# Kernel optimization log

Hardware: AMD Instinct MI355X
Metric: run time of the kernel (lower is better)

## Reference

```python
import math
import jax, jax.numpy as jnp
import numpy as np

D_MODEL = 1024
HID = 128
H, NB = 16, 16


def setup_inputs() -> dict:
    key = jax.random.key(0)
    ks = jax.random.split(key, 8)
    B, L = 4, 4096
    theta_path = jax.random.normal(ks[0], (B, L, H, NB), dtype=jnp.float32)
    content_emb = jax.random.normal(ks[1], (B, L, D_MODEL), dtype=jnp.float32)
    # measure_head params (PyTorch Linear default init: U(-1/sqrt(fan_in), 1/sqrt(fan_in)))
    s1 = 1.0 / math.sqrt(D_MODEL)
    s2 = 1.0 / math.sqrt(HID)
    W1 = jax.random.uniform(ks[2], (D_MODEL, HID), minval=-s1, maxval=s1, dtype=jnp.float32)
    b1 = jax.random.uniform(ks[3], (HID,), minval=-s1, maxval=s1, dtype=jnp.float32)
    W2 = jax.random.uniform(ks[4], (HID, H * NB), minval=-s2, maxval=s2, dtype=jnp.float32)
    b2 = jax.random.uniform(ks[5], (H * NB,), minval=-s2, maxval=s2, dtype=jnp.float32)
    log_Pi = jnp.zeros((H, NB), dtype=jnp.float32)
    log_R = jnp.zeros((H, NB), dtype=jnp.float32)
    return {"theta_path": theta_path, "content_emb": content_emb, "W1": W1, "b1": b1,
            "W2": W2, "b2": b2, "log_Pi": log_Pi, "log_R": log_R}


def _affine_scan(alpha, u):
    # d_t = alpha_t * d_{t-1} + u_t, d_0 = u_0 (zero initial state), scan over axis=1 (L)
    def combine(left, right):
        a_l, u_l = left
        a_r, u_r = right
        return a_l * a_r, a_r * u_l + u_r
    _, d = jax.lax.associative_scan(combine, (alpha, u), axis=1)
    return d


def reference(theta_path, content_emb, W1, b1, W2, b2, log_Pi, log_R):
    B, L, _, _ = theta_path.shape
    h = jax.nn.gelu(content_emb @ W1 + b1, approximate=False)  # [B,L,128], exact GELU as torch
    z = jnp.pi * jnp.tanh((h @ W2 + b2).reshape(B, L, H, NB))
    diff = z - theta_path
    nu = jnp.arctan2(jnp.sin(diff), jnp.cos(diff))  # wrapped angle residual
    Pi = jnp.exp(log_Pi)[None, None]  # [1,1,H,NB]
    R = jnp.exp(log_R)[None, None]
    K = Pi / jnp.maximum(Pi + R, 1e-08)
    Kf = jnp.broadcast_to(K, (B, L, H, NB))
    alpha = 1.0 - Kf
    u = Kf * nu
    d = _affine_scan(alpha, u)
    return (theta_path + d,
            jnp.broadcast_to(Pi, (B, L, H, NB)),
            Kf,
            jnp.broadcast_to(R, (B, L, H, NB)))
```

## Files before the change

### kernel.cpp

```cpp
#include <hip/hip_runtime.h>
#include <math.h>

#define MTOT  16384
#define DM    1024
#define HIDN  128
#define HNB   256
#define NBAT  4
#define CLK   32
#define NBLK  512
#define CPB   128

typedef _Float16 v8h __attribute__((ext_vector_type(8)));
typedef float    v4f __attribute__((ext_vector_type(4)));
#define MFMA16(a,b,c) __builtin_amdgcn_mfma_f32_16x16x32_f16((a),(b),(c),0,0,0)

#define W1TILE  16384
#define W2BASE  524288
#define W2TILE  32768
#define BLOB_BYTES 655360

#define RAWOFF 0
#define W1OFF  16384
#define HHOFF  0
#define HLOFF  8192
#define ZOFF   16384
#define SMEMSZ 65536

#define VMCNT_(N) asm volatile("s_waitcnt vmcnt(" #N ")" ::: "memory")
#define VMCNT(N) VMCNT_(N)
#define BARRIER() do { asm volatile("s_waitcnt lgkmcnt(0)" ::: "memory"); \
                       __builtin_amdgcn_s_barrier(); } while (0)

typedef const __attribute__((address_space(1))) void* gas1_t;
typedef __attribute__((address_space(3))) void* las3_t;

__device__ __forceinline__ void gld16(const void* g, void* l) {
    __builtin_amdgcn_global_load_lds((gas1_t)g, (las3_t)l, 16, 0, 0);
}

__global__ __launch_bounds__(256) void k_prep(
    const float* __restrict__ W1,
    const float* __restrict__ W2,
    char* __restrict__ blobs)
{
    __shared__ float lds[32][260];
    const int t = threadIdx.x, blk = blockIdx.x;
    if (blk < 32) {
        const int k0 = blk * 32;
        #pragma unroll
        for (int i = 0; i < 4; ++i) {
            int j = t + i * 256;
            int k = j >> 5, n4 = (j & 31) << 2;
            *(float4*)&lds[k][n4] = *(const float4*)&W1[(size_t)(k0 + k) * HIDN + n4];
        }
        __syncthreads();
        const int fl = t & 63, np = t >> 6;
        const int kb = (fl >> 4) * 8;
        #pragma unroll
        for (int fi = 0; fi < 2; ++fi) {
            const int col = 32 * np + 16 * fi + (fl & 15);
            union { _Float16 h[8]; int4 v; } H, L;
            #pragma unroll
            for (int e = 0; e < 8; ++e) {
                float v = lds[kb + e][col];
                _Float16 hh = (_Float16)v;
                H.h[e] = hh;
                L.h[e] = (_Float16)((v - (float)hh) * 4096.f);
            }
            char* d = blobs + blk * W1TILE + np * 2048 + fi * 1024 + fl * 16;
            *(int4*)d = H.v;
            *(int4*)(d + 8192) = L.v;
        }
    } else {
        const int ks = blk - 32, k0 = ks * 32;
        #pragma unroll
        for (int i = 0; i < 8; ++i) {
            int j = t + i * 256;
            int k = j >> 6, n4 = (j & 63) << 2;
            *(float4*)&lds[k][n4] = *(const float4*)&W2[(size_t)(k0 + k) * HNB + n4];
        }
        __syncthreads();
        const int fl = t & 63, cg0 = t >> 6;
        const int kb = (fl >> 4) * 8;
        #pragma unroll
        for (int i = 0; i < 4; ++i) {
            const int cg = cg0 * 4 + i;
            const int col = cg * 16 + (fl & 15);
            union { _Float16 h[8]; int4 v; } H, L;
            #pragma unroll
            for (int e = 0; e < 8; ++e) {
                float v = lds[kb + e][col];
                _Float16 hh = (_Float16)v;
                H.h[e] = hh;
                L.h[e] = (_Float16)((v - (float)hh) * 4096.f);
            }
            char* d = blobs + W2BASE + ks * W2TILE + cg * 1024 + fl * 16;
            *(int4*)d = H.v;
            *(int4*)(d + 16384) = L.v;
        }
    }
}

__global__ __launch_bounds__(512, 4) void k_mega(
    const float* __restrict__ A,
    const float* __restrict__ theta,
    const float* __restrict__ b1, const float* __restrict__ b2,
    const float* __restrict__ logPi, const float* __restrict__ logR,
    const char* __restrict__ blobs,
    float* __restrict__ out0, float* __restrict__ out2,
    float* fill1, float* fill3,
    float* carry, int cstride)
{
    __shared__ __attribute__((aligned(16))) char smem[SMEMSZ];

    const int tid  = threadIdx.x;
    const int blk  = blockIdx.x;
    const int m0   = blk * CLK;
    const int lane = tid & 63;
    const int wid  = tid >> 6;
    const int ln15 = lane & 15;
    const int q    = lane >> 4;
    const int np   = wid & 3;
    const int mh   = wid >> 2;

    const int mh_s = wid >> 1, half_s = wid & 1;
    const float* aSrc = A + (size_t)(m0 + 16 * mh_s + ln15) * DM + q * 8 + half_s * 4;
    const int rawDst = wid * 1024 + lane * 16;

    const int wq = wid & 3;
    const char* wSrc = blobs + wq * 2048 + (size_t)lane * 16;
    const int   wDst = wq * 2048 + lane * 16;

    v4f acc1[2], acc2[2];
    acc1[0] = acc1[1] = (v4f){0.f, 0.f, 0.f, 0.f};
    acc2[0] = acc2[1] = (v4f){0.f, 0.f, 0.f, 0.f};

#define STEP(KT, AV, WV, DO_RAW, DO_W) do { \
    if (wid < 4) { \
        if (DO_RAW) gld16(aSrc + (size_t)((KT) + 3) * 32, \
                          smem + RAWOFF + (((KT) + 3) & 3) * 4096 + rawDst); \
    } else if (DO_W) { \
        const char* ws_ = wSrc + (size_t)((KT) + 2) * W1TILE; \
        char* wd_ = smem + W1OFF + (((KT) + 2) % 3) * 16384 + wDst; \
        gld16(ws_, wd_);             gld16(ws_ + 1024, wd_ + 1024); \
        gld16(ws_ + 8192, wd_ + 8192); gld16(ws_ + 9216, wd_ + 9216); \
    } \
    { \
        const char* rawb = smem + RAWOFF + ((KT) & 3) * 4096 + mh * 2048 + lane * 16; \
        v4f lo = *(const v4f*)rawb; \
        v4f hi = *(const v4f*)(rawb + 1024); \
        const char* wbB = smem + W1OFF + ((KT) % 3) * 16384 + np * 2048 + lane * 16; \
        v8h wh0 = *(const v8h*)(wbB); \
        v8h wh1 = *(const v8h*)(wbB + 1024); \
        v8h wl0 = *(const v8h*)(wbB + 8192); \
        v8h wl1 = *(const v8h*)(wbB + 9216); \
        v8h ah, al; \
        _Pragma("unroll") \
        for (int e_ = 0; e_ < 4; ++e_) { \
            _Float16 t0_ = (_Float16)lo[e_]; \
            ah[e_] = t0_; \
            al[e_] = (_Float16)((lo[e_] - (float)t0_) * 4096.f); \
            _Float16 t1_ = (_Float16)hi[e_]; \
            ah[e_ + 4] = t1_; \
            al[e_ + 4] = (_Float16)((hi[e_] - (float)t1_) * 4096.f); \
        } \
        acc1[0] = MFMA16(ah, wh0, acc1[0]); \
        acc2[0] = MFMA16(ah, wl0, acc2[0]); \
        acc2[0] = MFMA16(al, wh0, acc2[0]); \
        acc1[1] = MFMA16(ah, wh1, acc1[1]); \
        acc2[1] = MFMA16(ah, wl1, acc2[1]); \
        acc2[1] = MFMA16(al, wh1, acc2[1]); \
    } \
    if (wid < 4) { VMCNT(AV); } else { VMCNT(WV); } \
    BARRIER(); \
} while (0)

    if (wid < 4) {
        gld16(aSrc,      smem + RAWOFF + 0 * 4096 + rawDst);
        gld16(aSrc + 32, smem + RAWOFF + 1 * 4096 + rawDst);
        gld16(aSrc + 64, smem + RAWOFF + 2 * 4096 + rawDst);
        VMCNT(2);
    } else {
        #pragma unroll
        for (int t2 = 0; t2 < 2; ++t2) {
            const char* ws_ = wSrc + (size_t)t2 * W1TILE;
            char* wd_ = smem + W1OFF + t2 * 16384 + wDst;
            gld16(ws_, wd_);               gld16(ws_ + 1024, wd_ + 1024);
            gld16(ws_ + 8192, wd_ + 8192); gld16(ws_ + 9216, wd_ + 9216);
        }
        VMCNT(4);
    }
    BARRIER();

    STEP(0,2,4,1,1);  STEP(1,2,4,1,1);  STEP(2,2,4,1,1);  STEP(3,2,4,1,1);
    STEP(4,2,4,1,1);  STEP(5,2,4,1,1);  STEP(6,2,4,1,1);  STEP(7,2,4,1,1);
    STEP(8,2,4,1,1);  STEP(9,2,4,1,1);  STEP(10,2,4,1,1); STEP(11,2,4,1,1);
    STEP(12,2,4,1,1); STEP(13,2,4,1,1); STEP(14,2,4,1,1); STEP(15,2,4,1,1);
    STEP(16,2,4,1,1); STEP(17,2,4,1,1); STEP(18,2,4,1,1); STEP(19,2,4,1,1);
    STEP(20,2,4,1,1); STEP(21,2,4,1,1); STEP(22,2,4,1,1); STEP(23,2,4,1,1);
    STEP(24,2,4,1,1); STEP(25,2,4,1,1); STEP(26,2,4,1,1); STEP(27,2,4,1,1);
    STEP(28,2,4,1,1); STEP(29,1,4,0,1); STEP(30,0,0,0,0); STEP(31,0,0,0,0);

    const float inv = 1.f / 4096.f;
    #pragma unroll
    for (int ni = 0; ni < 2; ++ni) {
        const int colH = 32 * np + 16 * ni + ln15;
        const float bv = b1[colH];
        const int qH = (colH >> 3) & 3;
        const int eH = colH & 7;
        #pragma unroll
        for (int r = 0; r < 4; ++r) {
            float y = acc1[ni][r] + acc2[ni][r] * inv + bv;
            float h = 0.5f * y * (1.f + erff(y * 0.70710678118654752f));
            _Float16 hh = (_Float16)h;
            _Float16 hl = (_Float16)((h - (float)hh) * 4096.f);
            const int fl = (4 * q + r) + 16 * qH;
            const int byte_ = mh * 4096 + np * 1024 + fl * 16 + eH * 2;
            *(_Float16*)(smem + HHOFF + byte_) = hh;
            *(_Float16*)(smem + HLOFF + byte_) = hl;
        }
    }
    BARRIER();

    v4f c1[4], c2[4];
    #pragma unroll
    for (int i = 0; i < 4; ++i) {
        c1[i] = (v4f){0.f, 0.f, 0.f, 0.f};
        c2[i] = (v4f){0.f, 0.f, 0.f, 0.f};
    }
    #pragma unroll
    for (int ks = 0; ks < 4; ++ks) {
        v8h hh = *(const v8h*)(smem + HHOFF + mh * 4096 + ks * 1024 + lane * 16);
        v8h hl = *(const v8h*)(smem + HLOFF + mh * 4096 + ks * 1024 + lane * 16);
        #pragma unroll
        for (int ni = 0; ni < 4; ++ni) {
            const char* wp = blobs + W2BASE + (size_t)ks * W2TILE
                           + (4 * np + ni) * 1024 + (size_t)lane * 16;
            v8h w2h = *(const v8h*)wp;
            v8h w2l = *(const v8h*)(wp + 16384);
            c1[ni] = MFMA16(hh, w2h, c1[ni]);
            c2[ni] = MFMA16(hh, w2l, c2[ni]);
            c2[ni] = MFMA16(hl, w2h, c2[ni]);
        }
    }

    #pragma unroll
    for (int ni = 0; ni < 4; ++ni) {
        const int col = 64 * np + 16 * ni + ln15;
        const float bv = b2[col];
        #pragma unroll
        for (int r = 0; r < 4; ++r) {
            const int row = 16 * mh + 4 * q + r;
            float y2 = c1[ni][r] + c2[ni][r] * inv + bv;
            *(float*)(smem + ZOFF + row * 1040 + col * 4) =
                3.14159265358979323846f * tanhf(y2);
        }
    }
    BARRIER();

    if (tid < 256) {
        const int c = tid;
        const float Pi = expf(logPi[c]);
        const float Rr = expf(logR[c]);
        const float Kc = Pi / fmaxf(Pi + Rr, 1e-8f);
        const float alpha = 1.f - Kc;
        float d = 0.f;
        float tv[2][16];
        #pragma unroll
        for (int i = 0; i < 16; ++i)
            tv[0][i] = theta[(size_t)(m0 + i) * HNB + c];
        #pragma unroll
        for (int g = 0; g < 2; ++g) {
            if (g < 1) {
                #pragma unroll
                for (int i = 0; i < 16; ++i)
                    tv[1][i] = theta[(size_t)(m0 + 16 + i) * HNB + c];
            }
            float sv[16];
            #pragma unroll
            for (int i = 0; i < 16; ++i) {
                float z = *(const float*)(smem + ZOFF + (g * 16 + i) * 1040 + c * 4);
                float diff = z - tv[g][i];
                float kq = rintf(diff * 0.15915494309189533577f);
                float nu = (float)((double)diff - (double)kq * 6.283185307179586476925286766559);
                d = fmaf(alpha, d, Kc * nu);
                sv[i] = tv[g][i] + d;
            }
            #pragma unroll
            for (int i = 0; i < 16; ++i)
                out0[(size_t)(m0 + g * 16 + i) * HNB + c] = sv[i];
        }
        carry[(size_t)blk * cstride + c] = d;
    } else {
        const int c = tid - 256;
        const float Pi = expf(logPi[c]);
        const float Rr = expf(logR[c]);
        const float Kc = Pi / fmaxf(Pi + Rr, 1e-8f);
        if (fill1) {
            #pragma unroll 4
            for (int i = 0; i < CLK; ++i) {
                size_t idx = (size_t)(m0 + i) * HNB + c;
                out2[idx]  = Kc;
                fill1[idx] = Pi;
                fill3[idx] = Rr;
            }
        } else {
            #pragma unroll 4
            for (int i = 0; i < CLK; ++i)
                out2[(size_t)(m0 + i) * HNB + c] = Kc;
        }
    }
#undef STEP
}

__global__ __launch_bounds__(256) void k_cscan(
    const float* __restrict__ logPi, const float* __restrict__ logR,
    float* carry, int cstride)
{
    const int c = threadIdx.x, b = blockIdx.x;
    const float Pi = expf(logPi[c]);
    const float Rr = expf(logR[c]);
    const float alpha = 1.f - Pi / fmaxf(Pi + Rr, 1e-8f);
    float A32 = alpha;
    #pragma unroll
    for (int i = 0; i < 5; ++i) A32 *= A32;
    float D = 0.f;
    for (int s0 = 0; s0 < CPB; s0 += 16) {
        float a[16];
        #pragma unroll
        for (int j = 0; j < 16; ++j)
            a[j] = carry[(size_t)(b * CPB + s0 + j) * cstride + c];
        #pragma unroll
        for (int j = 0; j < 16; ++j) {
            carry[(size_t)(b * CPB + s0 + j) * cstride + c] = D;
            D = fmaf(A32, D, a[j]);
        }
    }
}

__global__ __launch_bounds__(256) void k_apply(
    const float* __restrict__ logPi, const float* __restrict__ logR,
    float* __restrict__ out0, float* out1, float* out3,
    const float* carry, int cstride, int do_fills)
{
    const int blk = blockIdx.x;
    const int c = threadIdx.x;
    const float Pi = expf(logPi[c]);
    const float Rr = expf(logR[c]);
    const float Kc = Pi / fmaxf(Pi + Rr, 1e-8f);
    const float alpha = 1.f - Kc;
    float D = carry[(size_t)blk * cstride + c];
    float w = alpha * D;
    const size_t base = (size_t)blk * (CLK * HNB) + c;
    if (do_fills) {
        #pragma unroll 4
        for (int i = 0; i < CLK; ++i) {
            size_t idx = base + (size_t)i * HNB;
            out0[idx] += w;
            out1[idx] = Pi;
            out3[idx] = Rr;
            w *= alpha;
        }
    } else {
        #pragma unroll 4
        for (int i = 0; i < CLK; ++i) {
            size_t idx = base + (size_t)i * HNB;
            out0[idx] += w;
            w *= alpha;
        }
    }
}

extern "C" void kernel_launch(void* const* d_in, const int* in_sizes, int n_in,
                              void* d_out, int out_size, void* d_ws, size_t ws_size,
                              hipStream_t stream) {
    const float* theta   = (const float*)d_in[0];
    const float* content = (const float*)d_in[1];
    const float* W1      = (const float*)d_in[2];
    const float* b1      = (const float*)d_in[3];
    const float* W2      = (const float*)d_in[4];
    const float* b2      = (const float*)d_in[5];
    const float* logPi   = (const float*)d_in[6];
    const float* logR    = (const float*)d_in[7];

    float* out  = (float*)d_out;
    float* out0 = out;
    float* out1 = out + (size_t)MTOT * HNB;
    float* out2 = out + (size_t)2 * MTOT * HNB;
    float* out3 = out + (size_t)3 * MTOT * HNB;

    const size_t carry_bytes = (size_t)NBLK * 256 * 4;
    const size_t need = carry_bytes + BLOB_BYTES;
    float* carry; int cstride, do_fills; char* blobs;
    float *f1, *f3;
    if (ws_size >= need) {
        carry   = (float*)d_ws;
        cstride = 256;
        blobs   = (char*)d_ws + carry_bytes;
        f1 = out1; f3 = out3; do_fills = 0;
    } else {
        carry   = out3;
        cstride = CLK * HNB;
        blobs   = (char*)out1;
        f1 = nullptr; f3 = nullptr; do_fills = 1;
    }

    hipLaunchKernelGGL(k_prep, dim3(36), dim3(256), 0, stream, W1, W2, blobs);
    hipLaunchKernelGGL(k_mega, dim3(NBLK), dim3(512), 0, stream,
                       content, theta, b1, b2, logPi, logR, blobs,
                       out0, out2, f1, f3, carry, cstride);
    hipLaunchKernelGGL(k_cscan, dim3(NBAT), dim3(256), 0, stream,
                       logPi, logR, carry, cstride);
    hipLaunchKernelGGL(k_apply, dim3(NBLK), dim3(256), 0, stream,
                       logPi, logR, out0, out1, out3, carry, cstride, do_fills);
}
```

Baseline: 62.61 us.

## Double row-chunk to 64 and switch fused MLP to 32x32 MFMA tiles

Result: faster. 61.34 us (-2.0%).

```diff
diff --git a/kernel.cpp b/kernel.cpp
--- a/kernel.cpp
+++ b/kernel.cpp
@@ -6,25 +6,26 @@
 #define HIDN  128
 #define HNB   256
 #define NBAT  4
-#define CLK   32
-#define NBLK  512
-#define CPB   128
-
-typedef _Float16 v8h __attribute__((ext_vector_type(8)));
-typedef float    v4f __attribute__((ext_vector_type(4)));
-#define MFMA16(a,b,c) __builtin_amdgcn_mfma_f32_16x16x32_f16((a),(b),(c),0,0,0)
-
-#define W1TILE  16384
-#define W2BASE  524288
-#define W2TILE  32768
+#define CLK   64
+#define NBLK  256
+#define CPB   64
+
+typedef _Float16 v8h  __attribute__((ext_vector_type(8)));
+typedef float    v4f  __attribute__((ext_vector_type(4)));
+typedef float    v16f __attribute__((ext_vector_type(16)));
+#define MFMA32(a,b,c) __builtin_amdgcn_mfma_f32_32x32x16_f16((a),(b),(c),0,0,0)
+
+#define W1TILE 16384
+#define W2BASE 524288
+#define W2TILE 32768
 #define BLOB_BYTES 655360
 
 #define RAWOFF 0
-#define W1OFF  16384
+#define W1OFF  49152
 #define HHOFF  0
-#define HLOFF  8192
-#define ZOFF   16384
-#define SMEMSZ 65536
+#define HLOFF  16384
+#define ZOFF   49152
+#define SMEMSZ 115712
 
 #define VMCNT_(N) asm volatile("s_waitcnt vmcnt(" #N ")" ::: "memory")
 #define VMCNT(N) VMCNT_(N)
@@ -54,20 +55,18 @@
             *(float4*)&lds[k][n4] = *(const float4*)&W1[(size_t)(k0 + k) * HIDN + n4];
         }
         __syncthreads();
-        const int fl = t & 63, np = t >> 6;
-        const int kb = (fl >> 4) * 8;
-        #pragma unroll
-        for (int fi = 0; fi < 2; ++fi) {
-            const int col = 32 * np + 16 * fi + (fl & 15);
+        const int l = t & 63, fi = t >> 6;
+        #pragma unroll
+        for (int kb = 0; kb < 2; ++kb) {
             union { _Float16 h[8]; int4 v; } H, L;
             #pragma unroll
             for (int e = 0; e < 8; ++e) {
-                float v = lds[kb + e][col];
+                float v = lds[kb * 16 + (l >> 5) * 8 + e][32 * fi + (l & 31)];
                 _Float16 hh = (_Float16)v;
                 H.h[e] = hh;
                 L.h[e] = (_Float16)((v - (float)hh) * 4096.f);
             }
-            char* d = blobs + blk * W1TILE + np * 2048 + fi * 1024 + fl * 16;
+            char* d = blobs + blk * W1TILE + (fi * 2 + kb) * 1024 + l * 16;
             *(int4*)d = H.v;
             *(int4*)(d + 8192) = L.v;
         }
@@ -80,28 +79,29 @@
             *(float4*)&lds[k][n4] = *(const float4*)&W2[(size_t)(k0 + k) * HNB + n4];
         }
         __syncthreads();
-        const int fl = t & 63, cg0 = t >> 6;
-        const int kb = (fl >> 4) * 8;
-        #pragma unroll
-        for (int i = 0; i < 4; ++i) {
-            const int cg = cg0 * 4 + i;
-            const int col = cg * 16 + (fl & 15);
-            union { _Float16 h[8]; int4 v; } H, L;
+        const int l = t & 63, fi = t >> 6;
+        #pragma unroll
+        for (int jj = 0; jj < 2; ++jj) {
+            const int cg = fi * 2 + jj;
             #pragma unroll
-            for (int e = 0; e < 8; ++e) {
-                float v = lds[kb + e][col];
-                _Float16 hh = (_Float16)v;
-                H.h[e] = hh;
-                L.h[e] = (_Float16)((v - (float)hh) * 4096.f);
+            for (int kb = 0; kb < 2; ++kb) {
+                union { _Float16 h[8]; int4 v; } H, L;
+                #pragma unroll
+                for (int e = 0; e < 8; ++e) {
+                    float v = lds[kb * 16 + (l >> 5) * 8 + e][32 * cg + (l & 31)];
+                    _Float16 hh = (_Float16)v;
+                    H.h[e] = hh;
+                    L.h[e] = (_Float16)((v - (float)hh) * 4096.f);
+                }
+                char* d = blobs + W2BASE + ks * W2TILE + (cg * 2 + kb) * 1024 + l * 16;
+                *(int4*)d = H.v;
+                *(int4*)(d + 16384) = L.v;
             }
-            char* d = blobs + W2BASE + ks * W2TILE + cg * 1024 + fl * 16;
-            *(int4*)d = H.v;
-            *(int4*)(d + 16384) = L.v;
-        }
-    }
-}
-
-__global__ __launch_bounds__(512, 4) void k_mega(
+        }
+    }
+}
+
+__global__ __launch_bounds__(512, 2) void k_mega(
     const float* __restrict__ A,
     const float* __restrict__ theta,
     const float* __restrict__ b1, const float* __restrict__ b2,
@@ -118,140 +118,133 @@
     const int m0   = blk * CLK;
     const int lane = tid & 63;
     const int wid  = tid >> 6;
-    const int ln15 = lane & 15;
-    const int q    = lane >> 4;
+    const int c5   = lane & 31;
+    const int g    = lane >> 5;
     const int np   = wid & 3;
-    const int mh   = wid >> 2;
-
-    const int mh_s = wid >> 1, half_s = wid & 1;
-    const float* aSrc = A + (size_t)(m0 + 16 * mh_s + ln15) * DM + q * 8 + half_s * 4;
-    const int rawDst = wid * 1024 + lane * 16;
-
-    const int wq = wid & 3;
-    const char* wSrc = blobs + wq * 2048 + (size_t)lane * 16;
-    const int   wDst = wq * 2048 + lane * 16;
-
-    v4f acc1[2], acc2[2];
-    acc1[0] = acc1[1] = (v4f){0.f, 0.f, 0.f, 0.f};
-    acc2[0] = acc2[1] = (v4f){0.f, 0.f, 0.f, 0.f};
-
-#define STEP(KT, AV, WV, DO_RAW, DO_W) do { \
-    if (wid < 4) { \
-        if (DO_RAW) gld16(aSrc + (size_t)((KT) + 3) * 32, \
-                          smem + RAWOFF + (((KT) + 3) & 3) * 4096 + rawDst); \
-    } else if (DO_W) { \
-        const char* ws_ = wSrc + (size_t)((KT) + 2) * W1TILE; \
-        char* wd_ = smem + W1OFF + (((KT) + 2) % 3) * 16384 + wDst; \
-        gld16(ws_, wd_);             gld16(ws_ + 1024, wd_ + 1024); \
-        gld16(ws_ + 8192, wd_ + 8192); gld16(ws_ + 9216, wd_ + 9216); \
+    const int rh   = wid >> 2;
+
+    const int rh_s = wid >> 2, kb_s = (wid >> 1) & 1, half_s = wid & 1;
+    const float* aSrc = A + (size_t)(m0 + 32 * rh_s + c5) * DM
+                      + kb_s * 16 + g * 8 + half_s * 4;
+    const int rawPiece = wid * 1024 + lane * 16;
+
+    const char* wSrc = blobs + (size_t)wid * 4096 + (size_t)lane * 16;
+    const int   wDst = W1OFF + wid * 4096 + lane * 16;
+
+    v16f acc1, acc2;
+    #pragma unroll
+    for (int i = 0; i < 16; ++i) { acc1[i] = 0.f; acc2[i] = 0.f; }
+
+    gld16(aSrc,      smem + RAWOFF + 0 * 8192 + rawPiece);
+    gld16(aSrc + 32, smem + RAWOFF + 1 * 8192 + rawPiece);
+    #pragma unroll
+    for (int i = 0; i < 4; ++i)
+        gld16(wSrc + i * 1024, smem + wDst + i * 1024);
+    gld16(aSrc + 64, smem + RAWOFF + 2 * 8192 + rawPiece);
+    gld16(aSrc + 96, smem + RAWOFF + 3 * 8192 + rawPiece);
+    VMCNT(2);
+    BARRIER();
+
+#define PHASE(P) do { \
+    if ((P) <= 14) { \
+        const char* ws_ = wSrc + (size_t)(2 * (P) + 2) * W1TILE; \
+        char* wd_ = smem + (((P) + 1) & 1) * 32768 + wDst; \
+        gld16(ws_, wd_);               gld16(ws_ + 1024, wd_ + 1024); \
+        gld16(ws_ + 2048, wd_ + 2048); gld16(ws_ + 3072, wd_ + 3072); \
     } \
-    { \
-        const char* rawb = smem + RAWOFF + ((KT) & 3) * 4096 + mh * 2048 + lane * 16; \
-        v4f lo = *(const v4f*)rawb; \
-        v4f hi = *(const v4f*)(rawb + 1024); \
-        const char* wbB = smem + W1OFF + ((KT) % 3) * 16384 + np * 2048 + lane * 16; \
-        v8h wh0 = *(const v8h*)(wbB); \
-        v8h wh1 = *(const v8h*)(wbB + 1024); \
-        v8h wl0 = *(const v8h*)(wbB + 8192); \
-        v8h wl1 = *(const v8h*)(wbB + 9216); \
-        v8h ah, al; \
+    if ((P) <= 13) { \
+        gld16(aSrc + (size_t)(2 * (P) + 4) * 32, \
+              smem + RAWOFF + ((2 * (P) + 4) % 6) * 8192 + rawPiece); \
+        gld16(aSrc + (size_t)(2 * (P) + 5) * 32, \
+              smem + RAWOFF + ((2 * (P) + 5) % 6) * 8192 + rawPiece); \
+    } \
+    _Pragma("unroll") \
+    for (int t_ = 0; t_ < 2; ++t_) { \
+        const char* slot_ = smem + RAWOFF + ((2 * (P) + t_) % 6) * 8192; \
+        const char* wb_ = smem + W1OFF + ((P) & 1) * 32768 + t_ * 16384; \
         _Pragma("unroll") \
-        for (int e_ = 0; e_ < 4; ++e_) { \
-            _Float16 t0_ = (_Float16)lo[e_]; \
-            ah[e_] = t0_; \
-            al[e_] = (_Float16)((lo[e_] - (float)t0_) * 4096.f); \
-            _Float16 t1_ = (_Float16)hi[e_]; \
-            ah[e_ + 4] = t1_; \
-            al[e_ + 4] = (_Float16)((hi[e_] - (float)t1_) * 4096.f); \
+        for (int kb_ = 0; kb_ < 2; ++kb_) { \
+            v4f lo_ = *(const v4f*)(slot_ + (rh * 4 + kb_ * 2) * 1024 + lane * 16); \
+            v4f hi_ = *(const v4f*)(slot_ + (rh * 4 + kb_ * 2 + 1) * 1024 + lane * 16); \
+            v8h ah_, al_; \
+            _Pragma("unroll") \
+            for (int e_ = 0; e_ < 4; ++e_) { \
+                _Float16 t0_ = (_Float16)lo_[e_]; \
+                ah_[e_] = t0_; \
+                al_[e_] = (_Float16)((lo_[e_] - (float)t0_) * 4096.f); \
+                _Float16 t1_ = (_Float16)hi_[e_]; \
+                ah_[e_ + 4] = t1_; \
+                al_[e_ + 4] = (_Float16)((hi_[e_] - (float)t1_) * 4096.f); \
+            } \
+            v8h wh_ = *(const v8h*)(wb_ + (np * 2 + kb_) * 1024 + lane * 16); \
+            v8h wl_ = *(const v8h*)(wb_ + 8192 + (np * 2 + kb_) * 1024 + lane * 16); \
+            acc1 = MFMA32(ah_, wh_, acc1); \
+            acc2 = MFMA32(ah_, wl_, acc2); \
+            acc2 = MFMA32(al_, wh_, acc2); \
         } \
-        acc1[0] = MFMA16(ah, wh0, acc1[0]); \
-        acc2[0] = MFMA16(ah, wl0, acc2[0]); \
-        acc2[0] = MFMA16(al, wh0, acc2[0]); \
-        acc1[1] = MFMA16(ah, wh1, acc1[1]); \
-        acc2[1] = MFMA16(ah, wl1, acc2[1]); \
-        acc2[1] = MFMA16(al, wh1, acc2[1]); \
     } \
-    if (wid < 4) { VMCNT(AV); } else { VMCNT(WV); } \
+    if ((P) <= 13)      { VMCNT(2); } \
+    else if ((P) == 14) { VMCNT(0); } \
     BARRIER(); \
 } while (0)
 
-    if (wid < 4) {
-        gld16(aSrc,      smem + RAWOFF + 0 * 4096 + rawDst);
-        gld16(aSrc + 32, smem + RAWOFF + 1 * 4096 + rawDst);
-        gld16(aSrc + 64, smem + RAWOFF + 2 * 4096 + rawDst);
-        VMCNT(2);
-    } else {
-        #pragma unroll
-        for (int t2 = 0; t2 < 2; ++t2) {
-            const char* ws_ = wSrc + (size_t)t2 * W1TILE;
-            char* wd_ = smem + W1OFF + t2 * 16384 + wDst;
-            gld16(ws_, wd_);               gld16(ws_ + 1024, wd_ + 1024);
-            gld16(ws_ + 8192, wd_ + 8192); gld16(ws_ + 9216, wd_ + 9216);
-        }
-        VMCNT(4);
-    }
-    BARRIER();
-
-    STEP(0,2,4,1,1);  STEP(1,2,4,1,1);  STEP(2,2,4,1,1);  STEP(3,2,4,1,1);
-    STEP(4,2,4,1,1);  STEP(5,2,4,1,1);  STEP(6,2,4,1,1);  STEP(7,2,4,1,1);
-    STEP(8,2,4,1,1);  STEP(9,2,4,1,1);  STEP(10,2,4,1,1); STEP(11,2,4,1,1);
-    STEP(12,2,4,1,1); STEP(13,2,4,1,1); STEP(14,2,4,1,1); STEP(15,2,4,1,1);
-    STEP(16,2,4,1,1); STEP(17,2,4,1,1); STEP(18,2,4,1,1); STEP(19,2,4,1,1);
-    STEP(20,2,4,1,1); STEP(21,2,4,1,1); STEP(22,2,4,1,1); STEP(23,2,4,1,1);
-    STEP(24,2,4,1,1); STEP(25,2,4,1,1); STEP(26,2,4,1,1); STEP(27,2,4,1,1);
-    STEP(28,2,4,1,1); STEP(29,1,4,0,1); STEP(30,0,0,0,0); STEP(31,0,0,0,0);
+    PHASE(0);  PHASE(1);  PHASE(2);  PHASE(3);
+    PHASE(4);  PHASE(5);  PHASE(6);  PHASE(7);
+    PHASE(8);  PHASE(9);  PHASE(10); PHASE(11);
+    PHASE(12); PHASE(13); PHASE(14); PHASE(15);
+#undef PHASE
 
     const float inv = 1.f / 4096.f;
-    #pragma unroll
-    for (int ni = 0; ni < 2; ++ni) {
-        const int colH = 32 * np + 16 * ni + ln15;
-        const float bv = b1[colH];
-        const int qH = (colH >> 3) & 3;
-        const int eH = colH & 7;
-        #pragma unroll
-        for (int r = 0; r < 4; ++r) {
-            float y = acc1[ni][r] + acc2[ni][r] * inv + bv;
+    {
+        const int col = 32 * np + c5;
+        const float bv = b1[col];
+        const int kb2 = col >> 4;
+        const int fragBase = (rh * 8 + kb2) * 1024 + ((col & 15) >> 3) * 512
+                           + (col & 7) * 2;
+        #pragma unroll
+        for (int reg = 0; reg < 16; ++reg) {
+            const int row32 = (reg & 3) + 8 * (reg >> 2) + 4 * g;
+            float y = acc1[reg] + acc2[reg] * inv + bv;
             float h = 0.5f * y * (1.f + erff(y * 0.70710678118654752f));
             _Float16 hh = (_Float16)h;
             _Float16 hl = (_Float16)((h - (float)hh) * 4096.f);
-            const int fl = (4 * q + r) + 16 * qH;
-            const int byte_ = mh * 4096 + np * 1024 + fl * 16 + eH * 2;
-            *(_Float16*)(smem + HHOFF + byte_) = hh;
-            *(_Float16*)(smem + HLOFF + byte_) = hl;
+            *(_Float16*)(smem + HHOFF + fragBase + row32 * 16) = hh;
+            *(_Float16*)(smem + HLOFF + fragBase + row32 * 16) = hl;
         }
     }
     BARRIER();
 
-    v4f c1[4], c2[4];
-    #pragma unroll
-    for (int i = 0; i < 4; ++i) {
-        c1[i] = (v4f){0.f, 0.f, 0.f, 0.f};
-        c2[i] = (v4f){0.f, 0.f, 0.f, 0.f};
-    }
-    #pragma unroll
-    for (int ks = 0; ks < 4; ++ks) {
-        v8h hh = *(const v8h*)(smem + HHOFF + mh * 4096 + ks * 1024 + lane * 16);
-        v8h hl = *(const v8h*)(smem + HLOFF + mh * 4096 + ks * 1024 + lane * 16);
-        #pragma unroll
-        for (int ni = 0; ni < 4; ++ni) {
+    v16f d1[2], d2[2];
+    #pragma unroll
+    for (int i = 0; i < 16; ++i) {
+        d1[0][i] = 0.f; d1[1][i] = 0.f; d2[0][i] = 0.f; d2[1][i] = 0.f;
+    }
+    #pragma unroll
+    for (int kb2 = 0; kb2 < 8; ++kb2) {
+        v8h hh = *(const v8h*)(smem + HHOFF + (rh * 8 + kb2) * 1024 + lane * 16);
+        v8h hl = *(const v8h*)(smem + HLOFF + (rh * 8 + kb2) * 1024 + lane * 16);
+        const int ks = kb2 >> 1, kbl = kb2 & 1;
+        #pragma unroll
+        for (int ti = 0; ti < 2; ++ti) {
+            const int cg = np + ti * 4;
             const char* wp = blobs + W2BASE + (size_t)ks * W2TILE
-                           + (4 * np + ni) * 1024 + (size_t)lane * 16;
+                           + (cg * 2 + kbl) * 1024 + (size_t)lane * 16;
             v8h w2h = *(const v8h*)wp;
             v8h w2l = *(const v8h*)(wp + 16384);
-            c1[ni] = MFMA16(hh, w2h, c1[ni]);
-            c2[ni] = MFMA16(hh, w2l, c2[ni]);
-            c2[ni] = MFMA16(hl, w2h, c2[ni]);
-        }
-    }
-
-    #pragma unroll
-    for (int ni = 0; ni < 4; ++ni) {
-        const int col = 64 * np + 16 * ni + ln15;
+            d1[ti] = MFMA32(hh, w2h, d1[ti]);
+            d2[ti] = MFMA32(hh, w2l, d2[ti]);
+            d2[ti] = MFMA32(hl, w2h, d2[ti]);
+        }
+    }
+
+    #pragma unroll
+    for (int ti = 0; ti < 2; ++ti) {
+        const int col = 32 * (np + ti * 4) + c5;
         const float bv = b2[col];
         #pragma unroll
-        for (int r = 0; r < 4; ++r) {
-            const int row = 16 * mh + 4 * q + r;
-            float y2 = c1[ni][r] + c2[ni][r] * inv + bv;
+        for (int reg = 0; reg < 16; ++reg) {
+            const int row = 32 * rh + (reg & 3) + 8 * (reg >> 2) + 4 * g;
+            float y2 = d1[ti][reg] + d2[ti][reg] * inv + bv;
             *(float*)(smem + ZOFF + row * 1040 + col * 4) =
                 3.14159265358979323846f * tanhf(y2);
         }
@@ -270,25 +263,26 @@
         for (int i = 0; i < 16; ++i)
             tv[0][i] = theta[(size_t)(m0 + i) * HNB + c];
         #pragma unroll
-        for (int g = 0; g < 2; ++g) {
-            if (g < 1) {
+        for (int gr = 0; gr < 4; ++gr) {
+            const int cur = gr & 1;
+            if (gr < 3) {
                 #pragma unroll
                 for (int i = 0; i < 16; ++i)
-                    tv[1][i] = theta[(size_t)(m0 + 16 + i) * HNB + c];
+                    tv[cur ^ 1][i] = theta[(size_t)(m0 + (gr + 1) * 16 + i) * HNB + c];
             }
             float sv[16];
             #pragma unroll
             for (int i = 0; i < 16; ++i) {
-                float z = *(const float*)(smem + ZOFF + (g * 16 + i) * 1040 + c * 4);
-                float diff = z - tv[g][i];
+                float z = *(const float*)(smem + ZOFF + (gr * 16 + i) * 1040 + c * 4);
+                float diff = z - tv[cur][i];
                 float kq = rintf(diff * 0.15915494309189533577f);
                 float nu = (float)((double)diff - (double)kq * 6.283185307179586476925286766559);
                 d = fmaf(alpha, d, Kc * nu);
-                sv[i] = tv[g][i] + d;
+                sv[i] = tv[cur][i] + d;
             }
             #pragma unroll
             for (int i = 0; i < 16; ++i)
-                out0[(size_t)(m0 + g * 16 + i) * HNB + c] = sv[i];
+                out0[(size_t)(m0 + gr * 16 + i) * HNB + c] = sv[i];
         }
         carry[(size_t)blk * cstride + c] = d;
     } else {
@@ -310,7 +304,6 @@
                 out2[(size_t)(m0 + i) * HNB + c] = Kc;
         }
     }
-#undef STEP
 }
 
 __global__ __launch_bounds__(256) void k_cscan(
@@ -321,9 +314,9 @@
     const float Pi = expf(logPi[c]);
     const float Rr = expf(logR[c]);
     const float alpha = 1.f - Pi / fmaxf(Pi + Rr, 1e-8f);
-    float A32 = alpha;
-    #pragma unroll
-    for (int i = 0; i < 5; ++i) A32 *= A32;
+    float A64 = alpha;
+    #pragma unroll
+    for (int i = 0; i < 6; ++i) A64 *= A64;
     float D = 0.f;
     for (int s0 = 0; s0 < CPB; s0 += 16) {
         float a[16];
@@ -333,7 +326,7 @@
         #pragma unroll
         for (int j = 0; j < 16; ++j) {
             carry[(size_t)(b * CPB + s0 + j) * cstride + c] = D;
-            D = fmaf(A32, D, a[j]);
+            D = fmaf(A64, D, a[j]);
         }
     }
 }
```

## Fuse carry scan and apply into main kernel via decoupled-lookback flags

Applied to the files above, without the earlier changes.

New measurement: 102.2 us. 1.63x slower.

```diff
diff --git a/kernel.cpp b/kernel.cpp
--- a/kernel.cpp
+++ b/kernel.cpp
@@ -41,10 +41,14 @@
 __global__ __launch_bounds__(256) void k_prep(
     const float* __restrict__ W1,
     const float* __restrict__ W2,
-    char* __restrict__ blobs)
+    char* __restrict__ blobs,
+    int* flags)
 {
     __shared__ float lds[32][260];
     const int t = threadIdx.x, blk = blockIdx.x;
+    if (flags && blk < 2)
+        __hip_atomic_store(&flags[blk * 256 + t], 0, __ATOMIC_RELAXED,
+                           __HIP_MEMORY_SCOPE_AGENT);
     if (blk < 32) {
         const int k0 = blk * 32;
         #pragma unroll
@@ -109,7 +113,8 @@
     const char* __restrict__ blobs,
     float* __restrict__ out0, float* __restrict__ out2,
     float* fill1, float* fill3,
-    float* carry, int cstride)
+    float* carry, int cstride,
+    int* flags, int mode)
 {
     __shared__ __attribute__((aligned(16))) char smem[SMEMSZ];
 
@@ -200,6 +205,7 @@
     STEP(20,2,4,1,1); STEP(21,2,4,1,1); STEP(22,2,4,1,1); STEP(23,2,4,1,1);
     STEP(24,2,4,1,1); STEP(25,2,4,1,1); STEP(26,2,4,1,1); STEP(27,2,4,1,1);
     STEP(28,2,4,1,1); STEP(29,1,4,0,1); STEP(30,0,0,0,0); STEP(31,0,0,0,0);
+#undef STEP
 
     const float inv = 1.f / 4096.f;
     #pragma unroll
@@ -258,12 +264,13 @@
     }
     BARRIER();
 
+    float svr[CLK];
+    const int c = tid & 255;
+    const float Pi = expf(logPi[c]);
+    const float Rr = expf(logR[c]);
+    const float Kc = Pi / fmaxf(Pi + Rr, 1e-8f);
+    const float alpha = 1.f - Kc;
     if (tid < 256) {
-        const int c = tid;
-        const float Pi = expf(logPi[c]);
-        const float Rr = expf(logR[c]);
-        const float Kc = Pi / fmaxf(Pi + Rr, 1e-8f);
-        const float alpha = 1.f - Kc;
         float d = 0.f;
         float tv[2][16];
         #pragma unroll
@@ -276,7 +283,6 @@
                 for (int i = 0; i < 16; ++i)
                     tv[1][i] = theta[(size_t)(m0 + 16 + i) * HNB + c];
             }
-            float sv[16];
             #pragma unroll
             for (int i = 0; i < 16; ++i) {
                 float z = *(const float*)(smem + ZOFF + (g * 16 + i) * 1040 + c * 4);
@@ -284,18 +290,50 @@
                 float kq = rintf(diff * 0.15915494309189533577f);
                 float nu = (float)((double)diff - (double)kq * 6.283185307179586476925286766559);
                 d = fmaf(alpha, d, Kc * nu);
-                sv[i] = tv[g][i] + d;
-            }
-            #pragma unroll
-            for (int i = 0; i < 16; ++i)
-                out0[(size_t)(m0 + g * 16 + i) * HNB + c] = sv[i];
-        }
-        carry[(size_t)blk * cstride + c] = d;
+                svr[g * 16 + i] = tv[g][i] + d;
+            }
+        }
+        if (mode)
+            __hip_atomic_store(&carry[(size_t)blk * cstride + c], d,
+                               __ATOMIC_RELAXED, __HIP_MEMORY_SCOPE_AGENT);
+        else
+            carry[(size_t)blk * cstride + c] = d;
+    }
+    __syncthreads();
+    if (mode && tid == 0)
+        __hip_atomic_store(&flags[blk], 1, __ATOMIC_RELEASE,
+                           __HIP_MEMORY_SCOPE_AGENT);
+
+    if (tid < 256) {
+        if (mode) {
+            float A32 = alpha;
+            #pragma unroll
+            for (int i = 0; i < 5; ++i) A32 *= A32;
+            const int s  = blk & (CPB - 1);
+            const int bb = blk - s;
+            float D = 0.f, w = 1.f;
+            for (int j = s - 1; j >= 0; --j) {
+                while (__hip_atomic_load(&flags[bb + j], __ATOMIC_ACQUIRE,
+                                         __HIP_MEMORY_SCOPE_AGENT) == 0) {}
+                float cj = __hip_atomic_load(
+                    &carry[(size_t)(bb + j) * cstride + c],
+                    __ATOMIC_RELAXED, __HIP_MEMORY_SCOPE_AGENT);
+                D = fmaf(w, cj, D);
+                w *= A32;
+                if (__all(w < 1e-10f)) break;
+            }
+            float wo = alpha * D;
+            #pragma unroll
+            for (int i = 0; i < CLK; ++i) {
+                out0[(size_t)(m0 + i) * HNB + c] = svr[i] + wo;
+                wo *= alpha;
+            }
+        } else {
+            #pragma unroll
+            for (int i = 0; i < CLK; ++i)
+                out0[(size_t)(m0 + i) * HNB + c] = svr[i];
+        }
     } else {
-        const int c = tid - 256;
-        const float Pi = expf(logPi[c]);
-        const float Rr = expf(logR[c]);
-        const float Kc = Pi / fmaxf(Pi + Rr, 1e-8f);
         if (fill1) {
             #pragma unroll 4
             for (int i = 0; i < CLK; ++i) {
@@ -310,7 +348,6 @@
                 out2[(size_t)(m0 + i) * HNB + c] = Kc;
         }
     }
-#undef STEP
 }
 
 __global__ __launch_bounds__(256) void k_cscan(
@@ -341,7 +378,7 @@
 __global__ __launch_bounds__(256) void k_apply(
     const float* __restrict__ logPi, const float* __restrict__ logR,
     float* __restrict__ out0, float* out1, float* out3,
-    const float* carry, int cstride, int do_fills)
+    const float* carry, int cstride)
 {
     const int blk = blockIdx.x;
     const int c = threadIdx.x;
@@ -352,22 +389,13 @@
     float D = carry[(size_t)blk * cstride + c];
     float w = alpha * D;
     const size_t base = (size_t)blk * (CLK * HNB) + c;
-    if (do_fills) {
-        #pragma unroll 4
-        for (int i = 0; i < CLK; ++i) {
-            size_t idx = base + (size_t)i * HNB;
-            out0[idx] += w;
-            out1[idx] = Pi;
-            out3[idx] = Rr;
-            w *= alpha;
-        }
-    } else {
-        #pragma unroll 4
-        for (int i = 0; i < CLK; ++i) {
-            size_t idx = base + (size_t)i * HNB;
-            out0[idx] += w;
-            w *= alpha;
-        }
+    #pragma unroll 4
+    for (int i = 0; i < CLK; ++i) {
+        size_t idx = base + (size_t)i * HNB;
+        out0[idx] += w;
+        out1[idx] = Pi;
+        out3[idx] = Rr;
+        w *= alpha;
     }
 }
 
@@ -389,28 +417,32 @@
     float* out2 = out + (size_t)2 * MTOT * HNB;
     float* out3 = out + (size_t)3 * MTOT * HNB;
 
+    const size_t flag_bytes  = (size_t)NBLK * 4;
     const size_t carry_bytes = (size_t)NBLK * 256 * 4;
-    const size_t need = carry_bytes + BLOB_BYTES;
-    float* carry; int cstride, do_fills; char* blobs;
-    float *f1, *f3;
+    const size_t need = flag_bytes + carry_bytes + BLOB_BYTES;
+
     if (ws_size >= need) {
-        carry   = (float*)d_ws;
-        cstride = 256;
-        blobs   = (char*)d_ws + carry_bytes;
-        f1 = out1; f3 = out3; do_fills = 0;
+        int*   flags = (int*)d_ws;
+        float* carry = (float*)((char*)d_ws + flag_bytes);
+        char*  blobs = (char*)d_ws + flag_bytes + carry_bytes;
+        hipLaunchKernelGGL(k_prep, dim3(36), dim3(256), 0, stream,
+                           W1, W2, blobs, flags);
+        hipLaunchKernelGGL(k_mega, dim3(NBLK), dim3(512), 0, stream,
+                           content, theta, b1, b2, logPi, logR, blobs,
+                           out0, out2, out1, out3, carry, 256, flags, 1);
     } else {
-        carry   = out3;
-        cstride = CLK * HNB;
-        blobs   = (char*)out1;
-        f1 = nullptr; f3 = nullptr; do_fills = 1;
-    }
-
-    hipLaunchKernelGGL(k_prep, dim3(36), dim3(256), 0, stream, W1, W2, blobs);
-    hipLaunchKernelGGL(k_mega, dim3(NBLK), dim3(512), 0, stream,
-                       content, theta, b1, b2, logPi, logR, blobs,
-                       out0, out2, f1, f3, carry, cstride);
-    hipLaunchKernelGGL(k_cscan, dim3(NBAT), dim3(256), 0, stream,
-                       logPi, logR, carry, cstride);
-    hipLaunchKernelGGL(k_apply, dim3(NBLK), dim3(256), 0, stream,
-                       logPi, logR, out0, out1, out3, carry, cstride, do_fills);
-}
+        float* carry = out3;
+        int cstride  = CLK * HNB;
+        char* blobs  = (char*)out1;
+        hipLaunchKernelGGL(k_prep, dim3(36), dim3(256), 0, stream,
+                           W1, W2, blobs, (int*)nullptr);
+        hipLaunchKernelGGL(k_mega, dim3(NBLK), dim3(512), 0, stream,
+                           content, theta, b1, b2, logPi, logR, blobs,
+                           out0, out2, (float*)nullptr, (float*)nullptr,
+                           carry, cstride, (int*)nullptr, 0);
+        hipLaunchKernelGGL(k_cscan, dim3(NBAT), dim3(256), 0, stream,
+                           logPi, logR, carry, cstride);
+        hipLaunchKernelGGL(k_apply, dim3(NBLK), dim3(256), 0, stream,
+                           logPi, logR, out0, out1, out3, carry, cstride);
+    }
+}
```
